# Kernel tuning notes

Hardware: AMD Instinct MI355X
Metric: run time of the kernel (lower is better)

## Reference

```python
import jax, jax.numpy as jnp
import numpy as np

B, C, L = 32, 64, 2048
FREQ = L // 2 + 1            # 1025
BAND_SIZES = [341, 341, 343]  # freq//3, freq//3, remainder


def setup_inputs() -> dict:
    key = jax.random.key(0)
    k = jax.random.split(key, 6)
    X = jax.random.normal(k[0], (B, C, L), dtype=jnp.float32)
    A0 = jax.random.normal(k[1], (BAND_SIZES[0], BAND_SIZES[0]), dtype=jnp.float32)
    A1 = jax.random.normal(k[2], (BAND_SIZES[1], BAND_SIZES[1]), dtype=jnp.float32)
    A2 = jax.random.normal(k[3], (BAND_SIZES[2], BAND_SIZES[2]), dtype=jnp.float32)
    fusion_weights = jnp.ones((3,), dtype=jnp.float32)
    # Gumbel(0,1) noise for the 2-way gumbel-softmax over each (b, i, j) entry
    gumbel_noise = jax.random.gumbel(k[4], (B, C, C, 2), dtype=jnp.float32)
    return {"X": X, "A0": A0, "A1": A1, "A2": A2,
            "fusion_weights": fusion_weights, "gumbel_noise": gumbel_noise}


def _band_dist(band, A):
    # band: (b, c, s), A: (s, s). dist[b,i,j] = ||A (band_i - band_j)||^2
    # Gram trick: ||y_i - y_j||^2 = q_i + q_j - 2 y_i . y_j, y = band @ A^T
    Y = jnp.einsum('ds,bcs->bcd', A, band)          # (b, c, s)
    G = jnp.einsum('bid,bjd->bij', Y, Y)            # (b, c, c)
    q = jnp.einsum('bid,bid->bi', Y, Y)             # (b, c)
    dist = q[:, :, None] + q[:, None, :] - 2.0 * G
    return jnp.maximum(dist, 0.0)                   # guard fp round-off


def reference(X, A0, A1, A2, fusion_weights, gumbel_noise):
    XF = jnp.abs(jnp.fft.rfft(X, axis=-1))          # (b, c, FREQ)
    s0, s1, s2 = BAND_SIZES
    bands = (XF[..., :s0], XF[..., s0:s0 + s1], XF[..., s0 + s1:])
    As = (A0, A1, A2)
    dists = jnp.stack([_band_dist(b_, A_) for b_, A_ in zip(bands, As)], axis=-1)  # (b,c,c,3)
    w = jax.nn.softmax(fusion_weights)
    dist = jnp.einsum('bijk,k->bij', dists, w)      # (b, c, c)

    exp_dist = 1.0 / (dist + 1e-10)
    eye = jnp.eye(C, dtype=exp_dist.dtype)
    mask = 1.0 - eye
    exp_dist = exp_dist * mask
    exp_max = jax.lax.stop_gradient(jnp.max(exp_dist, axis=-1, keepdims=True))
    p = exp_dist / exp_max
    p = (p * mask + eye) * 0.99                     # probs in (0, 0.99]

    # Bernoulli via 2-class gumbel-softmax (hard, tau=1, straight-through)
    logits = jnp.stack([jnp.log(p / (1.0 - p)), jnp.log((1.0 - p) / p)], axis=-1)  # (b,c,c,2)
    y = logits + gumbel_noise
    y_soft = jax.nn.softmax(y, axis=-1)
    y_hard = jax.nn.one_hot(jnp.argmax(y, axis=-1), 2, dtype=y_soft.dtype)
    sample = (y_hard - jax.lax.stop_gradient(y_soft) + y_soft)[..., 0]  # (b,c,c)
    return sample[:, None, :, :]                    # (b, 1, c, c)
```

## Files before the change

### kernel.cpp

```cpp
#include <hip/hip_runtime.h>
#include <math.h>

#define Bn 32
#define Cn 64
#define Ln 2048
#define NFREQ 1025
#define S0c 341
#define S1c 341
#define S2c 343
#define KPAD 352
#define XROW (3 * 1056)
#define APLANE (3 * KPAD * KPAD)

#define PI_D 3.14159265358979323846

typedef double v4d __attribute__((ext_vector_type(4)));
typedef unsigned short u16;
typedef __attribute__((ext_vector_type(4))) u16 u16x4;
typedef __attribute__((ext_vector_type(8))) short short8;
typedef __attribute__((ext_vector_type(4))) float f32x4;

#define PADIX(i) ((i) + ((i) >> 4))

__device__ __forceinline__ u16 rneb(float f) {
    unsigned u = __float_as_uint(f);
    unsigned r = (u + 0x7FFFu + ((u >> 16) & 1u)) >> 16;
    return (u16)r;
}
__device__ __forceinline__ float b2f(u16 h) {
    return __uint_as_float(((unsigned)h) << 16);
}
__device__ __forceinline__ void split3(float v, u16& h1, u16& h2, u16& h3) {
    h1 = rneb(v);
    float r1 = v - b2f(h1);
    h2 = rneb(r1);
    float r2 = r1 - b2f(h2);
    h3 = rneb(r2);
}

__device__ __forceinline__ int rev4_10(unsigned x) {
    unsigned t = __brev(x) >> 22;
    return (int)(((t & 0x155u) << 1) | ((t >> 1) & 0x155u));
}

__global__ __launch_bounds__(256) void k_prep(const float* __restrict__ A0,
                                              const float* __restrict__ A1,
                                              const float* __restrict__ A2,
                                              float2* __restrict__ tw,
                                              u16* __restrict__ AS) {
    int b = blockIdx.x;
    int tid = threadIdx.x;
    if (b < 8) {
        int t = b * 256 + tid;
        double ang = -2.0 * PI_D * (double)t / 2048.0;
        double s, c;
        sincos(ang, &s, &c);
        tw[t] = make_float2((float)c, (float)s);
        return;
    }
    int i = b - 8;
    int z = i / 484;
    const float* A = (z == 0) ? A0 : ((z == 1) ? A1 : A2);
    int S = (z == 2) ? S2c : S0c;
    int idx = (i % 484) * 256 + tid;
    int d = idx / KPAD, kk = idx - d * KPAD;
    float v = (d < S && kk < S) ? A[(size_t)d * S + kk] : 0.0f;
    u16 h1, h2, h3;
    split3(v, h1, h2, h3);
    size_t o = ((size_t)z * KPAD + d) * KPAD + kk;
    AS[o] = h1;
    AS[APLANE + o] = h2;
    AS[2 * (size_t)APLANE + o] = h3;
}

__global__ __launch_bounds__(256) void k_fft(const float* __restrict__ X,
                                             const float2* __restrict__ tw,
                                             u16* __restrict__ XS) {
    __shared__ float re[1088];
    __shared__ float im[1088];
    int row = blockIdx.x;
    int tid = threadIdx.x;
    {
        int k = tid;
        float2 w1 = tw[2 * k];
        float2 w2 = tw[4 * k];
        float2 w3 = tw[6 * k];
        int i0 = PADIX(k), i1 = PADIX(k + 256), i2 = PADIX(k + 512), i3 = PADIX(k + 768);
        const float2* xr = (const float2*)(X + (size_t)row * Ln);
        float2 v0 = xr[k];
        float2 v1 = xr[k + 256];
        float2 v2 = xr[k + 512];
        float2 v3 = xr[k + 768];
        float ar = v0.x, ai = v0.y;
        float br = v1.x, bi = v1.y;
        float cr = v2.x, ci = v2.y;
        float dr = v3.x, di = v3.y;
        float t0r = ar + cr, t0i = ai + ci;
        float t1r = ar - cr, t1i = ai - ci;
        float t2r = br + dr, t2i = bi + di;
        float t3r = br - dr, t3i = bi - di;
        re[i0] = t0r + t2r; im[i0] = t0i + t2i;
        float u1r = t1r + t3i, u1i = t1i - t3r;
        re[i1] = u1r * w1.x - u1i * w1.y; im[i1] = u1r * w1.y + u1i * w1.x;
        float u2r = t0r - t2r, u2i = t0i - t2i;
        re[i2] = u2r * w2.x - u2i * w2.y; im[i2] = u2r * w2.y + u2i * w2.x;
        float u3r = t1r - t3i, u3i = t1i + t3r;
        re[i3] = u3r * w3.x - u3i * w3.y; im[i3] = u3r * w3.y + u3i * w3.x;
    }
    __syncthreads();
    #pragma unroll
    for (int s = 1; s < 5; ++s) {
        int log2Q = 8 - 2 * s;
        int Q = 1 << log2Q;
        int k = tid & (Q - 1);
        int g = tid >> log2Q;
        int base = (g << (log2Q + 2)) + k;
        int i0 = PADIX(base), i1 = PADIX(base + Q), i2 = PADIX(base + 2 * Q), i3 = PADIX(base + 3 * Q);
        int step = 2 << (2 * s);
        float2 w1 = tw[k * step];
        float2 w2 = tw[2 * k * step];
        float2 w3 = tw[3 * k * step];
        float ar = re[i0], ai = im[i0];
        float br = re[i1], bi = im[i1];
        float cr = re[i2], ci = im[i2];
        float dr = re[i3], di = im[i3];
        float t0r = ar + cr, t0i = ai + ci;
        float t1r = ar - cr, t1i = ai - ci;
        float t2r = br + dr, t2i = bi + di;
        float t3r = br - dr, t3i = bi - di;
        re[i0] = t0r + t2r; im[i0] = t0i + t2i;
        float u1r = t1r + t3i, u1i = t1i - t3r;
        re[i1] = u1r * w1.x - u1i * w1.y; im[i1] = u1r * w1.y + u1i * w1.x;
        float u2r = t0r - t2r, u2i = t0i - t2i;
        re[i2] = u2r * w2.x - u2i * w2.y; im[i2] = u2r * w2.y + u2i * w2.x;
        float u3r = t1r - t3i, u3i = t1i + t3r;
        re[i3] = u3r * w3.x - u3i * w3.y; im[i3] = u3r * w3.y + u3i * w3.x;
        __syncthreads();
    }
    u16* xrow = XS + (size_t)row * XROW;
    if (tid < 31) {
        int pp = (tid < 11) ? (341 + tid) : ((tid < 22) ? (682 + tid) : (1025 + tid));
        xrow[pp] = 0; xrow[1056 + pp] = 0; xrow[2112 + pp] = 0;
    }
    for (int k = tid; k <= 1024; k += 256) {
        float Xr, Xi;
        if (k == 0)        { Xr = re[0] + im[0]; Xi = 0.0f; }
        else if (k == 1024){ Xr = re[0] - im[0]; Xi = 0.0f; }
        else {
            int rv  = PADIX(rev4_10((unsigned)k));
            int rv2 = PADIX(rev4_10((unsigned)(1024 - k)));
            float2 t = tw[k];
            float Zr = re[rv],  Zi = im[rv];
            float Wr = re[rv2], Wi = im[rv2];
            float Er = 0.5f * (Zr + Wr), Ei = 0.5f * (Zi - Wi);
            float Or = 0.5f * (Zi + Wi), Oi = -0.5f * (Zr - Wr);
            Xr = Er + t.x * Or - t.y * Oi;
            Xi = Ei + t.x * Oi + t.y * Or;
        }
        float v = sqrtf(Xr * Xr + Xi * Xi);
        int zb = (k < S0c) ? 0 : ((k < S0c + S1c) ? 1 : 2);
        int pos = k + 11 * zb;
        u16 h1, h2, h3;
        split3(v, h1, h2, h3);
        xrow[pos] = h1;
        xrow[1056 + pos] = h2;
        xrow[2112 + pos] = h3;
    }
}

__global__ __launch_bounds__(256) void k_gemm(const u16* __restrict__ XS,
                                              const u16* __restrict__ AS,
                                              float* __restrict__ Y) {
    const int Sarr[3] = {S0c, S1c, S2c};
    const int Oarr[3] = {0, S0c, S0c + S1c};
    int z = blockIdx.z;
    int S = Sarr[z], O = Oarr[z];

    __shared__ u16 sX1[64][40], sX2[64][40], sX3[64][40];
    __shared__ u16 sA1[32][40], sA2[32][40], sA3[32][40];

    int r0 = blockIdx.x * 64;
    int d0 = blockIdx.y * 32;
    int tid = threadIdx.x;
    int lane = tid & 63, w = tid >> 6;
    int wm = (w >> 1) * 32, wn = (w & 1) * 16;
    int fm = lane & 15, kq = lane >> 4;
    int row8 = tid >> 3, seg4 = (tid & 7) * 4;

    f32x4 z4 = {0.0f, 0.0f, 0.0f, 0.0f};
    short8 aone, afm;
    {
        u16 hone = 0x3F80;
        u16 hfm = rneb((float)fm);
        #pragma unroll
        for (int j = 0; j < 8; ++j) { aone[j] = (short)hone; afm[j] = (short)hfm; }
    }
    f32x4 calR = __builtin_amdgcn_mfma_f32_16x16x32_bf16(afm, aone, z4, 0, 0, 0);
    f32x4 calC = __builtin_amdgcn_mfma_f32_16x16x32_bf16(aone, afm, z4, 0, 0, 0);
    int rIdx[4], cIdx[4];
    #pragma unroll
    for (int i = 0; i < 4; ++i) {
        rIdx[i] = (int)(calR[i] * 0.03125f + 0.5f);
        cIdx[i] = (int)(calC[i] * 0.03125f + 0.5f);
    }

    const u16* xb0 = XS + (size_t)(r0 + row8) * XROW + (size_t)z * KPAD + seg4;
    const u16* xb1 = xb0 + 32 * (size_t)XROW;
    const u16* ab  = AS + ((size_t)z * KPAD + (d0 + row8)) * KPAD + seg4;

    u16x4 wxa1, wxa2, wxa3, wxb1, wxb2, wxb3, wa1, wa2, wa3;
    auto load_tile = [&](int st) {
        int ko = st * 32;
        wxa1 = *(const u16x4*)(xb0 + ko);
        wxa2 = *(const u16x4*)(xb0 + 1056 + ko);
        wxa3 = *(const u16x4*)(xb0 + 2112 + ko);
        wxb1 = *(const u16x4*)(xb1 + ko);
        wxb2 = *(const u16x4*)(xb1 + 1056 + ko);
        wxb3 = *(const u16x4*)(xb1 + 2112 + ko);
        wa1  = *(const u16x4*)(ab + ko);
        wa2  = *(const u16x4*)(ab + APLANE + ko);
        wa3  = *(const u16x4*)(ab + 2 * (size_t)APLANE + ko);
    };

    double acc0[4] = {0.0, 0.0, 0.0, 0.0};
    double acc1[4] = {0.0, 0.0, 0.0, 0.0};
    load_tile(0);
    const int nsteps = KPAD / 32;
    for (int st = 0; st < nsteps; ++st) {
        __syncthreads();
        *(u16x4*)&sX1[row8][seg4] = wxa1;
        *(u16x4*)&sX2[row8][seg4] = wxa2;
        *(u16x4*)&sX3[row8][seg4] = wxa3;
        *(u16x4*)&sX1[row8 + 32][seg4] = wxb1;
        *(u16x4*)&sX2[row8 + 32][seg4] = wxb2;
        *(u16x4*)&sX3[row8 + 32][seg4] = wxb3;
        *(u16x4*)&sA1[row8][seg4] = wa1;
        *(u16x4*)&sA2[row8][seg4] = wa2;
        *(u16x4*)&sA3[row8][seg4] = wa3;
        __syncthreads();
        if (st + 1 < nsteps) load_tile(st + 1);
        short8 b1 = *(const short8*)&sA1[wn + fm][kq * 8];
        short8 b2 = *(const short8*)&sA2[wn + fm][kq * 8];
        short8 b3 = *(const short8*)&sA3[wn + fm][kq * 8];
        {
            short8 a1 = *(const short8*)&sX1[wm + fm][kq * 8];
            short8 a2 = *(const short8*)&sX2[wm + fm][kq * 8];
            short8 a3 = *(const short8*)&sX3[wm + fm][kq * 8];
            f32x4 p1 = __builtin_amdgcn_mfma_f32_16x16x32_bf16(a1, b1, z4, 0, 0, 0);
            f32x4 p2 = __builtin_amdgcn_mfma_f32_16x16x32_bf16(a1, b2, z4, 0, 0, 0);
            p2 = __builtin_amdgcn_mfma_f32_16x16x32_bf16(a2, b1, p2, 0, 0, 0);
            p2 = __builtin_amdgcn_mfma_f32_16x16x32_bf16(a1, b3, p2, 0, 0, 0);
            p2 = __builtin_amdgcn_mfma_f32_16x16x32_bf16(a2, b2, p2, 0, 0, 0);
            p2 = __builtin_amdgcn_mfma_f32_16x16x32_bf16(a3, b1, p2, 0, 0, 0);
            #pragma unroll
            for (int i = 0; i < 4; ++i) acc0[i] += (double)p1[i] + (double)p2[i];
        }
        {
            short8 a1 = *(const short8*)&sX1[wm + 16 + fm][kq * 8];
            short8 a2 = *(const short8*)&sX2[wm + 16 + fm][kq * 8];
            short8 a3 = *(const short8*)&sX3[wm + 16 + fm][kq * 8];
            f32x4 p1 = __builtin_amdgcn_mfma_f32_16x16x32_bf16(a1, b1, z4, 0, 0, 0);
            f32x4 p2 = __builtin_amdgcn_mfma_f32_16x16x32_bf16(a1, b2, z4, 0, 0, 0);
            p2 = __builtin_amdgcn_mfma_f32_16x16x32_bf16(a2, b1, p2, 0, 0, 0);
            p2 = __builtin_amdgcn_mfma_f32_16x16x32_bf16(a1, b3, p2, 0, 0, 0);
            p2 = __builtin_amdgcn_mfma_f32_16x16x32_bf16(a2, b2, p2, 0, 0, 0);
            p2 = __builtin_amdgcn_mfma_f32_16x16x32_bf16(a3, b1, p2, 0, 0, 0);
            #pragma unroll
            for (int i = 0; i < 4; ++i) acc1[i] += (double)p1[i] + (double)p2[i];
        }
    }
    #pragma unroll
    for (int i = 0; i < 4; ++i) {
        int d = d0 + wn + cIdx[i];
        if (d < S) {
            Y[(size_t)(r0 + wm + rIdx[i]) * NFREQ + O + d] = (float)acc0[i];
            Y[(size_t)(r0 + wm + 16 + rIdx[i]) * NFREQ + O + d] = (float)acc1[i];
        }
    }
}

__global__ __launch_bounds__(256) void k_dist(const float* __restrict__ Y,
                                              const float* __restrict__ fw,
                                              double* __restrict__ part) {
    __shared__ double sY[64][34];
    int b = blockIdx.x;
    int chunk = blockIdx.y;
    int dlo = chunk * 128;
    int dhi = (chunk == 7) ? NFREQ : dlo + 128;
    int tid = threadIdx.x;
    int lane = tid & 63, w = tid >> 6;
    int wm = (w >> 1) * 32, wn = (w & 1) * 32;
    int fm = lane & 15, kq = lane >> 4;
    int kl = tid & 31, rl = tid >> 5;

    double f0 = (double)fw[0], f1 = (double)fw[1], f2 = (double)fw[2];
    double m = fmax(f0, fmax(f1, f2));
    double e0 = exp(f0 - m), e1 = exp(f1 - m), e2 = exp(f2 - m);
    double esum = e0 + e1 + e2;
    double sw0 = sqrt(e0 / esum), sw1 = sqrt(e1 / esum), sw2 = sqrt(e2 / esum);

    v4d zero = {0.0, 0.0, 0.0, 0.0};
    double aval = (double)fm;
    v4d calR = __builtin_amdgcn_mfma_f64_16x16x4f64(aval, 1.0, zero, 0, 0, 0);
    v4d calC = __builtin_amdgcn_mfma_f64_16x16x4f64(1.0, aval, zero, 0, 0, 0);
    int rIdx[4], cIdx[4];
    #pragma unroll
    for (int i = 0; i < 4; ++i) {
        rIdx[i] = (int)(calR[i] * 0.25);
        cIdx[i] = (int)(calC[i] * 0.25);
    }

    const float* Yb = Y + (size_t)b * Cn * NFREQ;
    auto load_tile = [&](int k0, double* py) {
        int d = dlo + k0 + kl;
        bool dv = d < dhi;
        double sw = dv ? ((d < S0c) ? sw0 : ((d < S0c + S1c) ? sw1 : sw2)) : 0.0;
        #pragma unroll
        for (int i = 0; i < 8; ++i)
            py[i] = dv ? (double)Yb[(size_t)(rl + 8 * i) * NFREQ + d] * sw : 0.0;
    };

    v4d acc00 = zero, acc01 = zero, acc10 = zero, acc11 = zero;
    double py[8];
    load_tile(0, py);
    int nsteps = (dhi - dlo + 31) / 32;
    for (int st = 0; st < nsteps; ++st) {
        __syncthreads();
        #pragma unroll
        for (int i = 0; i < 8; ++i) sY[rl + 8 * i][kl] = py[i];
        __syncthreads();
        if (st + 1 < nsteps) load_tile((st + 1) * 32, py);
        #pragma unroll
        for (int t = 0; t < 8; ++t) {
            int k = 4 * t + kq;
            double a0 = sY[wm + fm][k];
            double a1 = sY[wm + 16 + fm][k];
            double b0 = sY[wn + fm][k];
            double b1 = sY[wn + 16 + fm][k];
            acc00 = __builtin_amdgcn_mfma_f64_16x16x4f64(a0, b0, acc00, 0, 0, 0);
            acc01 = __builtin_amdgcn_mfma_f64_16x16x4f64(a0, b1, acc01, 0, 0, 0);
            acc10 = __builtin_amdgcn_mfma_f64_16x16x4f64(a1, b0, acc10, 0, 0, 0);
            acc11 = __builtin_amdgcn_mfma_f64_16x16x4f64(a1, b1, acc11, 0, 0, 0);
        }
    }
    double* pb = part + (((size_t)b * 8 + chunk) << 12);
    #pragma unroll
    for (int i = 0; i < 4; ++i) {
        int rowA = wm + rIdx[i], rowB = rowA + 16;
        int cA = wn + cIdx[i], cB = cA + 16;
        pb[rowA * 64 + cA] = acc00[i];
        pb[rowA * 64 + cB] = acc01[i];
        pb[rowB * 64 + cA] = acc10[i];
        pb[rowB * 64 + cB] = acc11[i];
    }
}

__global__ __launch_bounds__(256) void k_decide(const double* __restrict__ part,
                                                const float* __restrict__ gum,
                                                float* __restrict__ out) {
    __shared__ double sQ[64];
    int b = blockIdx.x;
    int tid = threadIdx.x;
    const double* pb = part + (((size_t)b * 8) << 12);
    if (tid < 64) {
        double q = 0.0;
        #pragma unroll
        for (int c = 0; c < 8; ++c) q += pb[((size_t)c << 12) + tid * 65];
        sQ[tid] = q;
    }
    __syncthreads();
    int i = blockIdx.y * 4 + (tid >> 6);
    int j = tid & 63;
    double g = 0.0;
    #pragma unroll
    for (int c = 0; c < 8; ++c) g += pb[((size_t)c << 12) + i * 64 + j];
    double dist = fmax(sQ[i] + sQ[j] - 2.0 * g, 0.0);
    double e = (i == j) ? 0.0 : 1.0 / (dist + 1e-10);
    double emax = e;
    #pragma unroll
    for (int off = 32; off; off >>= 1)
        emax = fmax(emax, __shfl_xor(emax, off, 64));
    double p = (i == j) ? 0.99 : (e / emax) * 0.99;
    double l0 = log(p / (1.0 - p));
    double l1 = -l0;
    int idx = i * 64 + j;
    const float* gb = gum + (size_t)b * 8192;
    double y0 = l0 + (double)gb[2 * idx];
    double y1 = l1 + (double)gb[2 * idx + 1];
    out[(size_t)b * 4096 + idx] = (y0 >= y1) ? 1.0f : 0.0f;
}

extern "C" void kernel_launch(void* const* d_in, const int* in_sizes, int n_in,
                              void* d_out, int out_size, void* d_ws, size_t ws_size,
                              hipStream_t stream) {
    const float* X  = (const float*)d_in[0];
    const float* A0 = (const float*)d_in[1];
    const float* A1 = (const float*)d_in[2];
    const float* A2 = (const float*)d_in[3];
    const float* fw = (const float*)d_in[4];
    const float* gm = (const float*)d_in[5];
    float* out = (float*)d_out;

    char* ws = (char*)d_ws;
    float2* tw = (float2*)(ws);
    u16*  XS = (u16*)(ws + 32768);
    u16*  AS = (u16*)(ws + 13008896);
    float* Y = (float*)(ws + 15239168);
    double* part = (double*)(ws + 32768);

    k_prep<<<1460, 256, 0, stream>>>(A0, A1, A2, tw, AS);
    k_fft<<<Bn * Cn, 256, 0, stream>>>(X, tw, XS);
    k_gemm<<<dim3(32, 11, 3), 256, 0, stream>>>(XS, AS, Y);
    k_dist<<<dim3(Bn, 8), 256, 0, stream>>>(Y, fw, part);
    k_decide<<<dim3(Bn, 16), 256, 0, stream>>>(part, gm, out);
}
```

Measured before the change: 138.0 us.

## Fuse Gram and decision kernels using split-bf16 MFMA with in-block row norms

Merges the distance Gram kernel and the decision kernel into a single launch. Each block now covers one batch and a 16-row strip over the full frequency range, so the global partial-sum buffer and the cross-chunk reduction go away. The FP64 MFMA is replaced by three-way bf16-split MFMAs with double accumulation, and the row norms are computed directly in the load path. In exchange there is redundant loading of Y across the 4 strips, longer serial K loops with fewer blocks (128), and a possible precision change from the bf16 split.

```diff
diff --git a/kernel.cpp b/kernel.cpp
--- a/kernel.cpp
+++ b/kernel.cpp
@@ -14,7 +14,6 @@
 
 #define PI_D 3.14159265358979323846
 
-typedef double v4d __attribute__((ext_vector_type(4)));
 typedef unsigned short u16;
 typedef __attribute__((ext_vector_type(4))) u16 u16x4;
 typedef __attribute__((ext_vector_type(8))) short short8;
@@ -279,115 +278,128 @@
     }
 }
 
-__global__ __launch_bounds__(256) void k_dist(const float* __restrict__ Y,
-                                              const float* __restrict__ fw,
-                                              double* __restrict__ part) {
-    __shared__ double sY[64][34];
+__global__ __launch_bounds__(256) void k_distdecide(const float* __restrict__ Y,
+                                                    const float* __restrict__ fw,
+                                                    const float* __restrict__ gum,
+                                                    float* __restrict__ out) {
+    __shared__ u16 sY1[64][40], sY2[64][40], sY3[64][40];
+    __shared__ double sG[16][66];
+    __shared__ double qp[64][8];
+    __shared__ double qv[64];
+
     int b = blockIdx.x;
-    int chunk = blockIdx.y;
-    int dlo = chunk * 128;
-    int dhi = (chunk == 7) ? NFREQ : dlo + 128;
+    int s = blockIdx.y;
     int tid = threadIdx.x;
     int lane = tid & 63, w = tid >> 6;
-    int wm = (w >> 1) * 32, wn = (w & 1) * 32;
     int fm = lane & 15, kq = lane >> 4;
-    int kl = tid & 31, rl = tid >> 5;
+    int r = tid >> 3, seg = (tid & 7) * 4;
 
     double f0 = (double)fw[0], f1 = (double)fw[1], f2 = (double)fw[2];
     double m = fmax(f0, fmax(f1, f2));
     double e0 = exp(f0 - m), e1 = exp(f1 - m), e2 = exp(f2 - m);
     double esum = e0 + e1 + e2;
-    double sw0 = sqrt(e0 / esum), sw1 = sqrt(e1 / esum), sw2 = sqrt(e2 / esum);
-
-    v4d zero = {0.0, 0.0, 0.0, 0.0};
-    double aval = (double)fm;
-    v4d calR = __builtin_amdgcn_mfma_f64_16x16x4f64(aval, 1.0, zero, 0, 0, 0);
-    v4d calC = __builtin_amdgcn_mfma_f64_16x16x4f64(1.0, aval, zero, 0, 0, 0);
+    float sw0f = (float)sqrt(e0 / esum), sw1f = (float)sqrt(e1 / esum), sw2f = (float)sqrt(e2 / esum);
+
+    f32x4 z4 = {0.0f, 0.0f, 0.0f, 0.0f};
+    short8 aone, afm;
+    {
+        u16 hone = 0x3F80;
+        u16 hfm = rneb((float)fm);
+        #pragma unroll
+        for (int j = 0; j < 8; ++j) { aone[j] = (short)hone; afm[j] = (short)hfm; }
+    }
+    f32x4 calR = __builtin_amdgcn_mfma_f32_16x16x32_bf16(afm, aone, z4, 0, 0, 0);
+    f32x4 calC = __builtin_amdgcn_mfma_f32_16x16x32_bf16(aone, afm, z4, 0, 0, 0);
     int rIdx[4], cIdx[4];
     #pragma unroll
     for (int i = 0; i < 4; ++i) {
-        rIdx[i] = (int)(calR[i] * 0.25);
-        cIdx[i] = (int)(calC[i] * 0.25);
+        rIdx[i] = (int)(calR[i] * 0.03125f + 0.5f);
+        cIdx[i] = (int)(calC[i] * 0.03125f + 0.5f);
     }
 
     const float* Yb = Y + (size_t)b * Cn * NFREQ;
-    auto load_tile = [&](int k0, double* py) {
-        int d = dlo + k0 + kl;
-        bool dv = d < dhi;
-        double sw = dv ? ((d < S0c) ? sw0 : ((d < S0c + S1c) ? sw1 : sw2)) : 0.0;
-        #pragma unroll
-        for (int i = 0; i < 8; ++i)
-            py[i] = dv ? (double)Yb[(size_t)(rl + 8 * i) * NFREQ + d] * sw : 0.0;
+    double qa = 0.0, qb = 0.0;
+    u16x4 wa1, wa2, wa3, wb1, wb2, wb3;
+    auto load_tile = [&](int st) {
+        int k0 = st * 32 + seg;
+        #pragma unroll
+        for (int j = 0; j < 4; ++j) {
+            int d = k0 + j;
+            bool dv = d < NFREQ;
+            float sw = dv ? ((d < S0c) ? sw0f : ((d < S0c + S1c) ? sw1f : sw2f)) : 0.0f;
+            float va = dv ? Yb[(size_t)r * NFREQ + d] * sw : 0.0f;
+            float vb = dv ? Yb[(size_t)(r + 32) * NFREQ + d] * sw : 0.0f;
+            qa += (double)va * (double)va;
+            qb += (double)vb * (double)vb;
+            u16 h1, h2, h3;
+            split3(va, h1, h2, h3); wa1[j] = h1; wa2[j] = h2; wa3[j] = h3;
+            split3(vb, h1, h2, h3); wb1[j] = h1; wb2[j] = h2; wb3[j] = h3;
+        }
     };
 
-    v4d acc00 = zero, acc01 = zero, acc10 = zero, acc11 = zero;
-    double py[8];
-    load_tile(0, py);
-    int nsteps = (dhi - dlo + 31) / 32;
+    double acc[4] = {0.0, 0.0, 0.0, 0.0};
+    load_tile(0);
+    const int nsteps = 33;
     for (int st = 0; st < nsteps; ++st) {
         __syncthreads();
-        #pragma unroll
-        for (int i = 0; i < 8; ++i) sY[rl + 8 * i][kl] = py[i];
+        *(u16x4*)&sY1[r][seg] = wa1;
+        *(u16x4*)&sY2[r][seg] = wa2;
+        *(u16x4*)&sY3[r][seg] = wa3;
+        *(u16x4*)&sY1[r + 32][seg] = wb1;
+        *(u16x4*)&sY2[r + 32][seg] = wb2;
+        *(u16x4*)&sY3[r + 32][seg] = wb3;
         __syncthreads();
-        if (st + 1 < nsteps) load_tile((st + 1) * 32, py);
-        #pragma unroll
-        for (int t = 0; t < 8; ++t) {
-            int k = 4 * t + kq;
-            double a0 = sY[wm + fm][k];
-            double a1 = sY[wm + 16 + fm][k];
-            double b0 = sY[wn + fm][k];
-            double b1 = sY[wn + 16 + fm][k];
-            acc00 = __builtin_amdgcn_mfma_f64_16x16x4f64(a0, b0, acc00, 0, 0, 0);
-            acc01 = __builtin_amdgcn_mfma_f64_16x16x4f64(a0, b1, acc01, 0, 0, 0);
-            acc10 = __builtin_amdgcn_mfma_f64_16x16x4f64(a1, b0, acc10, 0, 0, 0);
-            acc11 = __builtin_amdgcn_mfma_f64_16x16x4f64(a1, b1, acc11, 0, 0, 0);
-        }
-    }
-    double* pb = part + (((size_t)b * 8 + chunk) << 12);
-    #pragma unroll
-    for (int i = 0; i < 4; ++i) {
-        int rowA = wm + rIdx[i], rowB = rowA + 16;
-        int cA = wn + cIdx[i], cB = cA + 16;
-        pb[rowA * 64 + cA] = acc00[i];
-        pb[rowA * 64 + cB] = acc01[i];
-        pb[rowB * 64 + cA] = acc10[i];
-        pb[rowB * 64 + cB] = acc11[i];
-    }
-}
-
-__global__ __launch_bounds__(256) void k_decide(const double* __restrict__ part,
-                                                const float* __restrict__ gum,
-                                                float* __restrict__ out) {
-    __shared__ double sQ[64];
-    int b = blockIdx.x;
-    int tid = threadIdx.x;
-    const double* pb = part + (((size_t)b * 8) << 12);
+        if (st + 1 < nsteps) load_tile(st + 1);
+        short8 a1 = *(const short8*)&sY1[s * 16 + fm][kq * 8];
+        short8 a2 = *(const short8*)&sY2[s * 16 + fm][kq * 8];
+        short8 a3 = *(const short8*)&sY3[s * 16 + fm][kq * 8];
+        short8 b1 = *(const short8*)&sY1[w * 16 + fm][kq * 8];
+        short8 b2 = *(const short8*)&sY2[w * 16 + fm][kq * 8];
+        short8 b3 = *(const short8*)&sY3[w * 16 + fm][kq * 8];
+        f32x4 p1 = __builtin_amdgcn_mfma_f32_16x16x32_bf16(a1, b1, z4, 0, 0, 0);
+        f32x4 p2 = __builtin_amdgcn_mfma_f32_16x16x32_bf16(a1, b2, z4, 0, 0, 0);
+        p2 = __builtin_amdgcn_mfma_f32_16x16x32_bf16(a2, b1, p2, 0, 0, 0);
+        p2 = __builtin_amdgcn_mfma_f32_16x16x32_bf16(a1, b3, p2, 0, 0, 0);
+        p2 = __builtin_amdgcn_mfma_f32_16x16x32_bf16(a2, b2, p2, 0, 0, 0);
+        p2 = __builtin_amdgcn_mfma_f32_16x16x32_bf16(a3, b1, p2, 0, 0, 0);
+        #pragma unroll
+        for (int i = 0; i < 4; ++i) acc[i] += (double)p1[i] + (double)p2[i];
+    }
+    #pragma unroll
+    for (int i = 0; i < 4; ++i)
+        sG[rIdx[i]][w * 16 + cIdx[i]] = acc[i];
+    qp[r][tid & 7] = qa;
+    qp[r + 32][tid & 7] = qb;
+    __syncthreads();
     if (tid < 64) {
         double q = 0.0;
         #pragma unroll
-        for (int c = 0; c < 8; ++c) q += pb[((size_t)c << 12) + tid * 65];
-        sQ[tid] = q;
+        for (int c = 0; c < 8; ++c) q += qp[tid][c];
+        qv[tid] = q;
     }
     __syncthreads();
-    int i = blockIdx.y * 4 + (tid >> 6);
-    int j = tid & 63;
-    double g = 0.0;
-    #pragma unroll
-    for (int c = 0; c < 8; ++c) g += pb[((size_t)c << 12) + i * 64 + j];
-    double dist = fmax(sQ[i] + sQ[j] - 2.0 * g, 0.0);
-    double e = (i == j) ? 0.0 : 1.0 / (dist + 1e-10);
-    double emax = e;
-    #pragma unroll
-    for (int off = 32; off; off >>= 1)
-        emax = fmax(emax, __shfl_xor(emax, off, 64));
-    double p = (i == j) ? 0.99 : (e / emax) * 0.99;
-    double l0 = log(p / (1.0 - p));
-    double l1 = -l0;
-    int idx = i * 64 + j;
+
     const float* gb = gum + (size_t)b * 8192;
-    double y0 = l0 + (double)gb[2 * idx];
-    double y1 = l1 + (double)gb[2 * idx + 1];
-    out[(size_t)b * 4096 + idx] = (y0 >= y1) ? 1.0f : 0.0f;
+    float* ob = out + (size_t)b * 4096;
+    #pragma unroll
+    for (int pass = 0; pass < 4; ++pass) {
+        int il = pass * 4 + (tid >> 6);
+        int i = s * 16 + il;
+        int j = tid & 63;
+        double g = sG[il][j];
+        double dist = fmax(qv[i] + qv[j] - 2.0 * g, 0.0);
+        double e = (i == j) ? 0.0 : 1.0 / (dist + 1e-10);
+        double emax = e;
+        #pragma unroll
+        for (int off = 32; off; off >>= 1)
+            emax = fmax(emax, __shfl_xor(emax, off, 64));
+        double p = (i == j) ? 0.99 : (e / emax) * 0.99;
+        double l0 = log(p / (1.0 - p));
+        int idx = i * 64 + j;
+        double y0 = l0 + (double)gb[2 * idx];
+        double y1 = -l0 + (double)gb[2 * idx + 1];
+        ob[idx] = (y0 >= y1) ? 1.0f : 0.0f;
+    }
 }
 
 extern "C" void kernel_launch(void* const* d_in, const int* in_sizes, int n_in,
@@ -406,11 +418,9 @@
     u16*  XS = (u16*)(ws + 32768);
     u16*  AS = (u16*)(ws + 13008896);
     float* Y = (float*)(ws + 15239168);
-    double* part = (double*)(ws + 32768);
 
     k_prep<<<1460, 256, 0, stream>>>(A0, A1, A2, tw, AS);
     k_fft<<<Bn * Cn, 256, 0, stream>>>(X, tw, XS);
     k_gemm<<<dim3(32, 11, 3), 256, 0, stream>>>(XS, AS, Y);
-    k_dist<<<dim3(Bn, 8), 256, 0, stream>>>(Y, fw, part);
-    k_decide<<<dim3(Bn, 16), 256, 0, stream>>>(part, gm, out);
-}
+    k_distdecide<<<dim3(Bn, 4), 256, 0, stream>>>(Y, fw, gm, out);
+}
```

Result: no change. 140.0 us (+1.5%).
